# Kernel tuning notes

Hardware: AMD Instinct MI355X
Metric: run time of the kernel (lower is better)

The kernel has to match this reference:

```python
import jax, jax.numpy as jnp
import numpy as np

N, E, D, L, R, G, C = 50000, 800000, 64, 3, 2, 128, 10


def setup_inputs() -> dict:
    key = jax.random.key(0)
    ks = jax.random.split(key, 16)
    s = 0.05
    x = jax.random.normal(ks[0], (N, D), dtype=jnp.float32)
    edge_index = jax.random.randint(ks[1], (2, E), 0, N, dtype=jnp.int64)
    edge_type = jax.random.randint(ks[2], (E,), 0, R, dtype=jnp.int64)
    batch = jnp.sort(jax.random.randint(ks[3], (N,), 0, G, dtype=jnp.int64))
    # per-layer self-loop Linear, per-(layer,relation) GIN eps + 2-layer MLP
    self_W = jax.random.normal(ks[4], (L, D, D), dtype=jnp.float32) * s
    self_b = jax.random.normal(ks[5], (L, D), dtype=jnp.float32) * s
    eps = jnp.zeros((L, R), dtype=jnp.float32)  # eps=0, train_eps=True
    mlp_W1 = jax.random.normal(ks[6], (L, R, D, D), dtype=jnp.float32) * s
    mlp_b1 = jax.random.normal(ks[7], (L, R, D), dtype=jnp.float32) * s
    mlp_W2 = jax.random.normal(ks[8], (L, R, D, D), dtype=jnp.float32) * s
    mlp_b2 = jax.random.normal(ks[9], (L, R, D), dtype=jnp.float32) * s
    lin1_W = jax.random.normal(ks[10], (D, D), dtype=jnp.float32) * s
    lin1_b = jax.random.normal(ks[11], (D,), dtype=jnp.float32) * s
    lin2_W = jax.random.normal(ks[12], (D, C), dtype=jnp.float32) * s
    lin2_b = jax.random.normal(ks[13], (C,), dtype=jnp.float32) * s
    return {"x": x, "edge_index": edge_index, "edge_type": edge_type, "batch": batch,
            "self_W": self_W, "self_b": self_b, "eps": eps,
            "mlp_W1": mlp_W1, "mlp_b1": mlp_b1, "mlp_W2": mlp_W2, "mlp_b2": mlp_b2,
            "lin1_W": lin1_W, "lin1_b": lin1_b, "lin2_W": lin2_W, "lin2_b": lin2_b}


def reference(x, edge_index, edge_type, batch, self_W, self_b, eps,
              mlp_W1, mlp_b1, mlp_W2, mlp_b2, lin1_W, lin1_b, lin2_W, lin2_b):
    src, dst = edge_index[0], edge_index[1]
    h = x
    for l in range(L):
        x_new = h @ self_W[l] + self_b[l]
        x_src = h[src]  # [E, D] gather of source features, done once per layer
        for r in range(R):
            # per-relation edge masking + scatter-add aggregation
            msg = jnp.where((edge_type == r)[:, None], x_src, jnp.zeros((), h.dtype))
            agg = jax.ops.segment_sum(msg, dst, num_segments=N)  # [N, D]
            z = (1.0 + eps[l, r]) * h + agg  # GIN combine
            z = jax.nn.relu(z @ mlp_W1[l, r] + mlp_b1[l, r])
            x_new = x_new + (z @ mlp_W2[l, r] + mlp_b2[l, r])
        h = x_new
    # global mean pooling over graphs
    sums = jax.ops.segment_sum(h, batch, num_segments=G)  # [G, D]
    counts = jax.ops.segment_sum(jnp.ones((N,), h.dtype), batch, num_segments=G)
    pooled = sums / jnp.maximum(counts, 1.0)[:, None]
    out = jax.nn.relu(pooled @ lin1_W + lin1_b)
    # dropout omitted (eval mode)
    out = out @ lin2_W + lin2_b
    return out
```

## Files before the change

### kernel.cpp

```cpp
#include <hip/hip_runtime.h>

#define Nn 50000
#define Dd 64
#define Ee 800000
#define Ll 3
#define Rr 2
#define Gg 128
#define Cc 10
#define NR (Nn * Rr)
#define NB ((NR + 1023) / 1024)
#define NT (Nn / 16)
#define EPAD (Ee + 4 * NR + 64)

#define CVT_B  3125
#define PREP_B 240
#define HIST_B 3125

typedef __attribute__((ext_vector_type(8))) short short8;
typedef __attribute__((ext_vector_type(4))) float f32x4;

__device__ __forceinline__ unsigned short bf16_rne(float x) {
  unsigned u = __float_as_uint(x);
  unsigned r = u + 0x7fffu + ((u >> 16) & 1u);
  return (unsigned short)(r >> 16);
}
__device__ __forceinline__ float bf16_tof(unsigned short b) {
  return __uint_as_float(((unsigned)b) << 16);
}
__device__ __forceinline__ void acc8(float* z, uint4 u) {
  z[0] += __uint_as_float(u.x << 16);
  z[1] += __uint_as_float(u.x & 0xffff0000u);
  z[2] += __uint_as_float(u.y << 16);
  z[3] += __uint_as_float(u.y & 0xffff0000u);
  z[4] += __uint_as_float(u.z << 16);
  z[5] += __uint_as_float(u.z & 0xffff0000u);
  z[6] += __uint_as_float(u.w << 16);
  z[7] += __uint_as_float(u.w & 0xffff0000u);
}

__global__ __launch_bounds__(256) void k_setup(
    const float* __restrict__ x, unsigned short* __restrict__ hb,
    const float* __restrict__ selfW, const float* __restrict__ W1,
    const float* __restrict__ W2, unsigned short* __restrict__ wtHi,
    unsigned short* __restrict__ wtLo,
    const int* __restrict__ dst, const int* __restrict__ et,
    int* __restrict__ counts)
{
  int b = blockIdx.x;
  if (b < CVT_B) {
    int i = b * 256 + threadIdx.x;
    const float4 v = *(const float4*)&x[(size_t)i * 4];
    ushort4 o;
    o.x = bf16_rne(v.x); o.y = bf16_rne(v.y);
    o.z = bf16_rne(v.z); o.w = bf16_rne(v.w);
    *(ushort4*)&hb[(size_t)i * 4] = o;
  } else if (b < CVT_B + PREP_B) {
    int i = (b - CVT_B) * 256 + threadIdx.x;
    int l = i / (5 * 4096);
    int rem = i - l * 5 * 4096;
    int m = rem >> 12;
    int e = rem & 4095;
    int k = e >> 6, c = e & 63;
    const float* p;
    if (m == 0)      p = selfW + (size_t)l * 4096;
    else if (m == 1) p = W1 + ((size_t)l * 2 + 0) * 4096;
    else if (m == 2) p = W2 + ((size_t)l * 2 + 0) * 4096;
    else if (m == 3) p = W1 + ((size_t)l * 2 + 1) * 4096;
    else             p = W2 + ((size_t)l * 2 + 1) * 4096;
    float w = p[e];
    unsigned short hi = bf16_rne(w);
    unsigned short lo = bf16_rne(w - bf16_tof(hi));
    size_t o = ((size_t)(l * 5 + m) * 64 + c) * 64 + k;
    wtHi[o] = hi;
    wtLo[o] = lo;
  } else {
    int e = (b - CVT_B - PREP_B) * 256 + threadIdx.x;
    atomicAdd(&counts[et[e] * Nn + dst[e]], 1);
  }
}

__global__ __launch_bounds__(1024) void k_scan1(
    const int* __restrict__ counts, int* __restrict__ offs,
    int* __restrict__ btot)
{
  __shared__ int s[1024];
  int i = blockIdx.x * 1024 + threadIdx.x;
  int v = (i < NR) ? ((counts[i] + 3) & ~3) : 0;
  s[threadIdx.x] = v;
  __syncthreads();
#pragma unroll
  for (int d = 1; d < 1024; d <<= 1) {
    int t = (threadIdx.x >= d) ? s[threadIdx.x - d] : 0;
    __syncthreads();
    s[threadIdx.x] += t;
    __syncthreads();
  }
  if (i < NR) offs[i + 1] = s[threadIdx.x];
  if (threadIdx.x == 1023) btot[blockIdx.x] = s[1023];
}

__global__ __launch_bounds__(128) void k_scan2(
    const int* __restrict__ btot, int* __restrict__ bscan)
{
  __shared__ int s[128];
  int v = (threadIdx.x < NB) ? btot[threadIdx.x] : 0;
  s[threadIdx.x] = v;
  __syncthreads();
#pragma unroll
  for (int d = 1; d < 128; d <<= 1) {
    int t = (threadIdx.x >= d) ? s[threadIdx.x - d] : 0;
    __syncthreads();
    s[threadIdx.x] += t;
    __syncthreads();
  }
  if (threadIdx.x < NB) bscan[threadIdx.x] = s[threadIdx.x] - v;
}

__global__ __launch_bounds__(1024) void k_scan3(
    const int* __restrict__ counts, const int* __restrict__ bscan,
    int* __restrict__ offs, int* __restrict__ cursor)
{
  int i = blockIdx.x * 1024 + threadIdx.x;
  if (i >= NR) return;
  int o = offs[i + 1] + bscan[blockIdx.x];
  offs[i + 1] = o;
  cursor[i] = o - ((counts[i] + 3) & ~3);
  if (i == 0) offs[0] = 0;
}

__global__ __launch_bounds__(256) void k_fill(
    const int* __restrict__ src, const int* __restrict__ dst,
    const int* __restrict__ et, int* __restrict__ cursor,
    int* __restrict__ elist)
{
  int e = blockIdx.x * 256 + threadIdx.x;
  if (e >= Ee) return;
  int pos = atomicAdd(&cursor[et[e] * Nn + dst[e]], 1);
  elist[pos] = src[e];
}

#define WOFF(m, c, ks) ((size_t)(m)*4096 + (size_t)(c)*64 + (ks)*32 + koff)

__global__ __launch_bounds__(128, 5) void k_update(
    const float* __restrict__ h, const unsigned short* __restrict__ hb,
    const int* __restrict__ offs, const int* __restrict__ counts,
    const int* __restrict__ elist,
    const unsigned short* __restrict__ wtHi, const unsigned short* __restrict__ wtLo,
    const float* __restrict__ selfb, const float* __restrict__ eps,
    const float* __restrict__ b1, const float* __restrict__ b2,
    float* __restrict__ hn, unsigned short* __restrict__ hnb, int l)
{
  __shared__ __align__(16) unsigned short tbh[2][16 * 72];
  __shared__ __align__(16) unsigned short tbl[2][16 * 72];
  float* xfer = (float*)&tbh[0][0];
  const int wave = threadIdx.x >> 6;
  const int lane = threadIdx.x & 63;
  const int task = blockIdx.x;
  const int r = wave;
  const int idx15 = lane & 15;
  const int kg = lane >> 4;
  const int koff = kg * 8;
  const int nodeA = task * 16 + idx15;

  float f[2][8];
  {
    const float* hp = &h[(size_t)nodeA * 64 + koff];
    const float4 a0 = *(const float4*)(hp);
    const float4 a1 = *(const float4*)(hp + 4);
    const float4 b0 = *(const float4*)(hp + 32);
    const float4 b1v = *(const float4*)(hp + 36);
    f[0][0] = a0.x; f[0][1] = a0.y; f[0][2] = a0.z; f[0][3] = a0.w;
    f[0][4] = a1.x; f[0][5] = a1.y; f[0][6] = a1.z; f[0][7] = a1.w;
    f[1][0] = b0.x; f[1][1] = b0.y; f[1][2] = b0.z; f[1][3] = b0.w;
    f[1][4] = b1v.x; f[1][5] = b1v.y; f[1][6] = b1v.z; f[1][7] = b1v.w;
  }

  const unsigned short* whi = wtHi + (size_t)l * 5 * 4096;
  const unsigned short* wlo = wtLo + (size_t)l * 5 * 4096;
  const int m1 = 1 + 2 * r, m2 = 2 + 2 * r;
  const float er = 1.0f + eps[l * Rr + r];

  float za[2][8];
#pragma unroll
  for (int ks = 0; ks < 2; ++ks)
#pragma unroll
    for (int jj = 0; jj < 8; ++jj) za[ks][jj] = 0.0f;
  {
    const int aidx = r * Nn + nodeA;
    const int jb = offs[aidx];
    const int je = jb + counts[aidx];
    int j = jb;
    if (j + 3 < je) {
      int4 ec = *(const int4*)&elist[j];
      for (; j + 3 < je; j += 4) {
        int4 en = *(const int4*)&elist[j + 4];
        const unsigned short* q0 = &hb[(size_t)ec.x * 64 + koff];
        const unsigned short* q1 = &hb[(size_t)ec.y * 64 + koff];
        const unsigned short* q2 = &hb[(size_t)ec.z * 64 + koff];
        const unsigned short* q3 = &hb[(size_t)ec.w * 64 + koff];
        const uint4 a0 = *(const uint4*)(q0);
        const uint4 a1 = *(const uint4*)(q1);
        const uint4 a2 = *(const uint4*)(q2);
        const uint4 a3 = *(const uint4*)(q3);
        const uint4 b0 = *(const uint4*)(q0 + 32);
        const uint4 b1q = *(const uint4*)(q1 + 32);
        const uint4 b2q = *(const uint4*)(q2 + 32);
        const uint4 b3 = *(const uint4*)(q3 + 32);
        acc8(za[0], a0); acc8(za[0], a1); acc8(za[0], a2); acc8(za[0], a3);
        acc8(za[1], b0); acc8(za[1], b1q); acc8(za[1], b2q); acc8(za[1], b3);
        ec = en;
      }
    }
    for (; j < je; ++j) {
      const unsigned short* q = &hb[(size_t)elist[j] * 64 + koff];
      const uint4 a = *(const uint4*)(q);
      const uint4 b = *(const uint4*)(q + 32);
      acc8(za[0], a); acc8(za[1], b);
    }
  }

  short8 zhi[2], zlo[2];
#pragma unroll
  for (int ks = 0; ks < 2; ++ks)
#pragma unroll
    for (int jj = 0; jj < 8; ++jj) {
      float zf = er * f[ks][jj] + za[ks][jj];
      unsigned short hb2 = bf16_rne(zf);
      zhi[ks][jj] = (short)hb2;
      zlo[ks][jj] = (short)bf16_rne(zf - bf16_tof(hb2));
    }

  f32x4 tacc[4];
#pragma unroll
  for (int cb = 0; cb < 4; ++cb) {
    float bi = b1[((size_t)l * 2 + r) * 64 + cb * 16 + idx15];
    tacc[cb] = (f32x4){bi, bi, bi, bi};
  }
#pragma unroll
  for (int cb = 0; cb < 4; ++cb) {
    int c = cb * 16 + idx15;
#pragma unroll
    for (int ks = 0; ks < 2; ++ks) {
      const short8 bh = *(const short8*)&whi[WOFF(m1, c, ks)];
      const short8 bl = *(const short8*)&wlo[WOFF(m1, c, ks)];
      tacc[cb] = __builtin_amdgcn_mfma_f32_16x16x32_bf16(zhi[ks], bh, tacc[cb], 0, 0, 0);
      tacc[cb] = __builtin_amdgcn_mfma_f32_16x16x32_bf16(zhi[ks], bl, tacc[cb], 0, 0, 0);
      tacc[cb] = __builtin_amdgcn_mfma_f32_16x16x32_bf16(zlo[ks], bh, tacc[cb], 0, 0, 0);
    }
  }
#pragma unroll
  for (int cb = 0; cb < 4; ++cb)
#pragma unroll
    for (int q = 0; q < 4; ++q) {
      float tv = fmaxf(tacc[cb][q], 0.0f);
      unsigned short hb2 = bf16_rne(tv);
      tbh[wave][(kg * 4 + q) * 72 + cb * 16 + idx15] = hb2;
      tbl[wave][(kg * 4 + q) * 72 + cb * 16 + idx15] = bf16_rne(tv - bf16_tof(hb2));
    }
  asm volatile("s_waitcnt lgkmcnt(0)" ::: "memory");
  __builtin_amdgcn_sched_barrier(0);
  short8 thi[2], tlo[2];
#pragma unroll
  for (int ks = 0; ks < 2; ++ks) {
    thi[ks] = *(const short8*)&tbh[wave][idx15 * 72 + ks * 32 + koff];
    tlo[ks] = *(const short8*)&tbl[wave][idx15 * 72 + ks * 32 + koff];
  }

  f32x4 facc[4];
#pragma unroll
  for (int cb = 0; cb < 4; ++cb) {
    int c = cb * 16 + idx15;
    float bi = b2[((size_t)l * 2 + r) * 64 + c];
    if (wave == 1) bi += selfb[l * 64 + c];
    facc[cb] = (f32x4){bi, bi, bi, bi};
  }
#pragma unroll
  for (int cb = 0; cb < 4; ++cb) {
    int c = cb * 16 + idx15;
#pragma unroll
    for (int ks = 0; ks < 2; ++ks) {
      const short8 bh = *(const short8*)&whi[WOFF(m2, c, ks)];
      const short8 bl = *(const short8*)&wlo[WOFF(m2, c, ks)];
      facc[cb] = __builtin_amdgcn_mfma_f32_16x16x32_bf16(thi[ks], bh, facc[cb], 0, 0, 0);
      facc[cb] = __builtin_amdgcn_mfma_f32_16x16x32_bf16(thi[ks], bl, facc[cb], 0, 0, 0);
      facc[cb] = __builtin_amdgcn_mfma_f32_16x16x32_bf16(tlo[ks], bh, facc[cb], 0, 0, 0);
    }
  }
  if (wave == 1) {
    short8 ahi[2], alo[2];
#pragma unroll
    for (int ks = 0; ks < 2; ++ks)
#pragma unroll
      for (int jj = 0; jj < 8; ++jj) {
        unsigned short hb2 = bf16_rne(f[ks][jj]);
        ahi[ks][jj] = (short)hb2;
        alo[ks][jj] = (short)bf16_rne(f[ks][jj] - bf16_tof(hb2));
      }
#pragma unroll
    for (int cb = 0; cb < 4; ++cb) {
      int c = cb * 16 + idx15;
#pragma unroll
      for (int ks = 0; ks < 2; ++ks) {
        const short8 bh = *(const short8*)&whi[WOFF(0, c, ks)];
        const short8 bl = *(const short8*)&wlo[WOFF(0, c, ks)];
        facc[cb] = __builtin_amdgcn_mfma_f32_16x16x32_bf16(ahi[ks], bh, facc[cb], 0, 0, 0);
        facc[cb] = __builtin_amdgcn_mfma_f32_16x16x32_bf16(ahi[ks], bl, facc[cb], 0, 0, 0);
        facc[cb] = __builtin_amdgcn_mfma_f32_16x16x32_bf16(alo[ks], bh, facc[cb], 0, 0, 0);
      }
    }
  }
  __syncthreads();
  if (wave == 1) {
#pragma unroll
    for (int cb = 0; cb < 4; ++cb)
#pragma unroll
      for (int q = 0; q < 4; ++q)
        xfer[(kg * 4 + q) * 65 + cb * 16 + idx15] = facc[cb][q];
  }
  __syncthreads();
  if (wave == 0) {
#pragma unroll
    for (int cb = 0; cb < 4; ++cb)
#pragma unroll
      for (int q = 0; q < 4; ++q) {
        int row = kg * 4 + q, col = cb * 16 + idx15;
        float v = facc[cb][q] + xfer[row * 65 + col];
        size_t o = ((size_t)task * 16 + row) * 64 + col;
        hn[o] = v;
        hnb[o] = bf16_rne(v);
      }
  }
}

__global__ __launch_bounds__(64) void k_poolhead(
    const float* __restrict__ h, const int* __restrict__ batch,
    const float* __restrict__ l1W, const float* __restrict__ l1b,
    const float* __restrict__ l2W, const float* __restrict__ l2b,
    float* __restrict__ out)
{
  int g = blockIdx.x;
  int lane = threadIdx.x;
  int lo = 0, hi = Nn;
  while (lo < hi) { int mid = (lo + hi) >> 1; if (batch[mid] < g) lo = mid + 1; else hi = mid; }
  int start = lo;
  hi = Nn;
  while (lo < hi) { int mid = (lo + hi) >> 1; if (batch[mid] < g + 1) lo = mid + 1; else hi = mid; }
  int end = lo;

  float acc = 0.0f;
  int i = start;
  for (; i + 3 < end; i += 4) {
    float v0 = h[(size_t)i * 64 + lane];
    float v1 = h[(size_t)(i + 1) * 64 + lane];
    float v2 = h[(size_t)(i + 2) * 64 + lane];
    float v3 = h[(size_t)(i + 3) * 64 + lane];
    acc += (v0 + v1) + (v2 + v3);
  }
  for (; i < end; ++i) acc += h[(size_t)i * 64 + lane];
  float p = acc / fmaxf((float)(end - start), 1.0f);

  float t = l1b[lane];
#pragma unroll
  for (int k = 0; k < Dd; ++k)
    t += __shfl(p, k, 64) * l1W[k * Dd + lane];
  t = fmaxf(t, 0.0f);
  float o = (lane < Cc) ? l2b[lane] : 0.0f;
#pragma unroll
  for (int k = 0; k < Dd; ++k) {
    float w = (lane < Cc) ? l2W[k * Cc + lane] : 0.0f;
    o += __shfl(t, k, 64) * w;
  }
  if (lane < Cc) out[(size_t)g * Cc + lane] = o;
}

extern "C" void kernel_launch(void* const* d_in, const int* in_sizes, int n_in,
                              void* d_out, int out_size, void* d_ws, size_t ws_size,
                              hipStream_t stream)
{
  const float* x     = (const float*)d_in[0];
  const int*   ei    = (const int*)d_in[1];
  const int*   et    = (const int*)d_in[2];
  const int*   batch = (const int*)d_in[3];
  const float* selfW = (const float*)d_in[4];
  const float* selfb = (const float*)d_in[5];
  const float* eps   = (const float*)d_in[6];
  const float* W1    = (const float*)d_in[7];
  const float* b1    = (const float*)d_in[8];
  const float* W2    = (const float*)d_in[9];
  const float* b2    = (const float*)d_in[10];
  const float* l1W   = (const float*)d_in[11];
  const float* l1b   = (const float*)d_in[12];
  const float* l2W   = (const float*)d_in[13];
  const float* l2b   = (const float*)d_in[14];
  float* out = (float*)d_out;

  float* buf0 = (float*)d_ws;
  float* buf1 = buf0 + (size_t)Nn * Dd;
  unsigned short* hb0 = (unsigned short*)(buf1 + (size_t)Nn * Dd);
  unsigned short* hb1 = hb0 + (size_t)Nn * Dd;
  unsigned short* wtHi = hb1 + (size_t)Nn * Dd;
  unsigned short* wtLo = wtHi + (size_t)Ll * 5 * 4096;
  int* counts = (int*)(wtLo + (size_t)Ll * 5 * 4096);
  int* offs   = counts + NR;
  int* cursor = offs + NR + 1;
  int* btot   = cursor + NR;
  int* bscan  = btot + NB;
  int* elist  = (int*)((((uintptr_t)(bscan + NB)) + 15) & ~(uintptr_t)15);

  const int* src = ei;
  const int* dst = ei + Ee;

  hipMemsetAsync(counts, 0, (size_t)NR * sizeof(int), stream);
  k_setup<<<CVT_B + PREP_B + HIST_B, 256, 0, stream>>>(
      x, hb0, selfW, W1, W2, wtHi, wtLo, dst, et, counts);

  k_scan1<<<NB, 1024, 0, stream>>>(counts, offs, btot);
  k_scan2<<<1, 128, 0, stream>>>(btot, bscan);
  k_scan3<<<NB, 1024, 0, stream>>>(counts, bscan, offs, cursor);
  k_fill<<<(Ee + 255) / 256, 256, 0, stream>>>(src, dst, et, cursor, elist);

  const float* h = x;
  const unsigned short* hbc = hb0;
  float* hn = buf0;
  unsigned short* hnb = hb1;
  for (int l = 0; l < Ll; ++l) {
    k_update<<<NT, 128, 0, stream>>>(h, hbc, offs, counts, elist, wtHi, wtLo,
                                     selfb, eps, b1, b2, hn, hnb, l);
    h = hn;
    hbc = hnb;
    hn = (hn == buf0) ? buf1 : buf0;
    hnb = (hnb == hb0) ? hb1 : hb0;
  }
  k_poolhead<<<Gg, 64, 0, stream>>>(h, batch, l1W, l1b, l2W, l2b, out);
}
```

Baseline: 296.5 us.

## Merge block-total scan into scan3, unroll edge gather by eight, relax occupancy

```diff
diff --git a/kernel.cpp b/kernel.cpp
--- a/kernel.cpp
+++ b/kernel.cpp
@@ -99,30 +99,25 @@
   if (threadIdx.x == 1023) btot[blockIdx.x] = s[1023];
 }
 
-__global__ __launch_bounds__(128) void k_scan2(
-    const int* __restrict__ btot, int* __restrict__ bscan)
-{
-  __shared__ int s[128];
+__global__ __launch_bounds__(1024) void k_scan3(
+    const int* __restrict__ counts, const int* __restrict__ btot,
+    int* __restrict__ offs, int* __restrict__ cursor)
+{
+  __shared__ int bs[128];
   int v = (threadIdx.x < NB) ? btot[threadIdx.x] : 0;
-  s[threadIdx.x] = v;
+  if (threadIdx.x < 128) bs[threadIdx.x] = v;
   __syncthreads();
 #pragma unroll
   for (int d = 1; d < 128; d <<= 1) {
-    int t = (threadIdx.x >= d) ? s[threadIdx.x - d] : 0;
+    int t = (threadIdx.x >= d && threadIdx.x < 128) ? bs[threadIdx.x - d] : 0;
     __syncthreads();
-    s[threadIdx.x] += t;
+    if (threadIdx.x < 128) bs[threadIdx.x] += t;
     __syncthreads();
   }
-  if (threadIdx.x < NB) bscan[threadIdx.x] = s[threadIdx.x] - v;
-}
-
-__global__ __launch_bounds__(1024) void k_scan3(
-    const int* __restrict__ counts, const int* __restrict__ bscan,
-    int* __restrict__ offs, int* __restrict__ cursor)
-{
+  int myb = (blockIdx.x == 0) ? 0 : bs[blockIdx.x - 1];
   int i = blockIdx.x * 1024 + threadIdx.x;
   if (i >= NR) return;
-  int o = offs[i + 1] + bscan[blockIdx.x];
+  int o = offs[i + 1] + myb;
   offs[i + 1] = o;
   cursor[i] = o - ((counts[i] + 3) & ~3);
   if (i == 0) offs[0] = 0;
@@ -141,7 +136,7 @@
 
 #define WOFF(m, c, ks) ((size_t)(m)*4096 + (size_t)(c)*64 + (ks)*32 + koff)
 
-__global__ __launch_bounds__(128, 5) void k_update(
+__global__ __launch_bounds__(128, 4) void k_update(
     const float* __restrict__ h, const unsigned short* __restrict__ hb,
     const int* __restrict__ offs, const int* __restrict__ counts,
     const int* __restrict__ elist,
@@ -190,26 +185,60 @@
     const int jb = offs[aidx];
     const int je = jb + counts[aidx];
     int j = jb;
-    if (j + 3 < je) {
-      int4 ec = *(const int4*)&elist[j];
-      for (; j + 3 < je; j += 4) {
-        int4 en = *(const int4*)&elist[j + 4];
-        const unsigned short* q0 = &hb[(size_t)ec.x * 64 + koff];
-        const unsigned short* q1 = &hb[(size_t)ec.y * 64 + koff];
-        const unsigned short* q2 = &hb[(size_t)ec.z * 64 + koff];
-        const unsigned short* q3 = &hb[(size_t)ec.w * 64 + koff];
+    if (j + 7 < je) {
+      int4 ec0 = *(const int4*)&elist[j];
+      int4 ec1 = *(const int4*)&elist[j + 4];
+      for (; j + 7 < je; j += 8) {
+        int4 en0 = *(const int4*)&elist[j + 8];
+        int4 en1 = *(const int4*)&elist[j + 12];
+        const unsigned short* q0 = &hb[(size_t)ec0.x * 64 + koff];
+        const unsigned short* q1 = &hb[(size_t)ec0.y * 64 + koff];
+        const unsigned short* q2 = &hb[(size_t)ec0.z * 64 + koff];
+        const unsigned short* q3 = &hb[(size_t)ec0.w * 64 + koff];
+        const unsigned short* q4 = &hb[(size_t)ec1.x * 64 + koff];
+        const unsigned short* q5 = &hb[(size_t)ec1.y * 64 + koff];
+        const unsigned short* q6 = &hb[(size_t)ec1.z * 64 + koff];
+        const unsigned short* q7 = &hb[(size_t)ec1.w * 64 + koff];
         const uint4 a0 = *(const uint4*)(q0);
         const uint4 a1 = *(const uint4*)(q1);
         const uint4 a2 = *(const uint4*)(q2);
         const uint4 a3 = *(const uint4*)(q3);
+        const uint4 a4 = *(const uint4*)(q4);
+        const uint4 a5 = *(const uint4*)(q5);
+        const uint4 a6 = *(const uint4*)(q6);
+        const uint4 a7 = *(const uint4*)(q7);
         const uint4 b0 = *(const uint4*)(q0 + 32);
         const uint4 b1q = *(const uint4*)(q1 + 32);
         const uint4 b2q = *(const uint4*)(q2 + 32);
         const uint4 b3 = *(const uint4*)(q3 + 32);
+        const uint4 b4 = *(const uint4*)(q4 + 32);
+        const uint4 b5 = *(const uint4*)(q5 + 32);
+        const uint4 b6 = *(const uint4*)(q6 + 32);
+        const uint4 b7 = *(const uint4*)(q7 + 32);
         acc8(za[0], a0); acc8(za[0], a1); acc8(za[0], a2); acc8(za[0], a3);
+        acc8(za[0], a4); acc8(za[0], a5); acc8(za[0], a6); acc8(za[0], a7);
         acc8(za[1], b0); acc8(za[1], b1q); acc8(za[1], b2q); acc8(za[1], b3);
-        ec = en;
+        acc8(za[1], b4); acc8(za[1], b5); acc8(za[1], b6); acc8(za[1], b7);
+        ec0 = en0; ec1 = en1;
       }
+    }
+    if (j + 3 < je) {
+      int4 ec = *(const int4*)&elist[j];
+      const unsigned short* q0 = &hb[(size_t)ec.x * 64 + koff];
+      const unsigned short* q1 = &hb[(size_t)ec.y * 64 + koff];
+      const unsigned short* q2 = &hb[(size_t)ec.z * 64 + koff];
+      const unsigned short* q3 = &hb[(size_t)ec.w * 64 + koff];
+      const uint4 a0 = *(const uint4*)(q0);
+      const uint4 a1 = *(const uint4*)(q1);
+      const uint4 a2 = *(const uint4*)(q2);
+      const uint4 a3 = *(const uint4*)(q3);
+      const uint4 b0 = *(const uint4*)(q0 + 32);
+      const uint4 b1q = *(const uint4*)(q1 + 32);
+      const uint4 b2q = *(const uint4*)(q2 + 32);
+      const uint4 b3 = *(const uint4*)(q3 + 32);
+      acc8(za[0], a0); acc8(za[0], a1); acc8(za[0], a2); acc8(za[0], a3);
+      acc8(za[1], b0); acc8(za[1], b1q); acc8(za[1], b2q); acc8(za[1], b3);
+      j += 4;
     }
     for (; j < je; ++j) {
       const unsigned short* q = &hb[(size_t)elist[j] * 64 + koff];
@@ -404,8 +433,7 @@
   int* offs   = counts + NR;
   int* cursor = offs + NR + 1;
   int* btot   = cursor + NR;
-  int* bscan  = btot + NB;
-  int* elist  = (int*)((((uintptr_t)(bscan + NB)) + 15) & ~(uintptr_t)15);
+  int* elist  = (int*)((((uintptr_t)(btot + NB)) + 15) & ~(uintptr_t)15);
 
   const int* src = ei;
   const int* dst = ei + Ee;
@@ -415,8 +443,7 @@
       x, hb0, selfW, W1, W2, wtHi, wtLo, dst, et, counts);
 
   k_scan1<<<NB, 1024, 0, stream>>>(counts, offs, btot);
-  k_scan2<<<1, 128, 0, stream>>>(btot, bscan);
-  k_scan3<<<NB, 1024, 0, stream>>>(counts, bscan, offs, cursor);
+  k_scan3<<<NB, 1024, 0, stream>>>(counts, btot, offs, cursor);
   k_fill<<<(Ee + 255) / 256, 256, 0, stream>>>(src, dst, et, cursor, elist);
 
   const float* h = x;
```

New measurement: 291.9 us. No clear change (-1.5%).
